# Kernel optimization log

Hardware: AMD Instinct MI355X
Metric: run time of the kernel (lower is better)

Reference implementation:

```python
import jax, jax.numpy as jnp
import numpy as np

B, C = 8, 8
IMG_H, IMG_W = 512, 1280
MAXDISP = (12, 3, 3)
CH3D = (16, 4, 4)          # channels_3d * growth_rate[i]
LAYERS_3D = 4
BASELINE, FOCAL = 0.2, 320.0
MIN_DEPTH, MAX_DEPTH = 0.1, 100.0


def _conv3d(x, w):
    # x: [B,Cin,D,H,W], w: [Cout,Cin,3,3,3], stride 1, padding 1 -> SAME
    return jax.lax.conv_general_dilated(
        x, w, (1, 1, 1), 'SAME',
        dimension_numbers=('NCDHW', 'OIDHW', 'NCDHW'))


def post_3dconv(cost, w_in, w_mid, w_out):
    # cost: [B,1,D,H,W]; conv->relu stack, final conv back to 1 channel
    x = jax.nn.relu(_conv3d(cost, w_in))
    for k in range(w_mid.shape[0]):
        x = jax.nn.relu(_conv3d(x, w_mid[k]))
    return _conv3d(x, w_out)


def build_volume_2d(fl, fr, maxdisp):
    # L1 cost volume: cost[b,d,h,w] = sum_c |fl[...,w] - fr[...,w-d]|, fr zero-padded left
    Bn, Cn, H, W = fl.shape
    d = jnp.arange(maxdisp)
    src = jnp.arange(W)[None, :] - d[:, None]              # [D,W]
    valid = (src >= 0).astype(fl.dtype)
    fr_s = jnp.take(fr, jnp.clip(src, 0, W - 1), axis=3)   # [B,C,H,D,W]
    fr_s = fr_s * valid[None, None, None]
    cost = jnp.abs(fl[:, :, :, None, :] - fr_s).sum(1)     # [B,H,D,W]
    return jnp.transpose(cost, (0, 2, 1, 3))               # [B,D,H,W]


def build_volume_2d3(fl, fr, maxdisp, disp):
    # residual cost volume around current disparity; warp == horizontal bilinear
    # sampling of fr at x - (disp - shift) with zero padding
    Bn, Cn, H, W = fl.shape
    shifts = jnp.arange(-maxdisp + 1, maxdisp, dtype=fl.dtype)      # [S]
    sd = disp[:, 0][:, None] - shifts[None, :, None, None]          # [B,S,H,W]
    xs = jnp.arange(W, dtype=fl.dtype)[None, None, None, :] - sd   # [B,S,H,W]
    x0 = jnp.floor(xs)
    w1 = xs - x0
    x0i = x0.astype(jnp.int32)

    def sample(xi):
        inb = ((xi >= 0) & (xi <= W - 1)).astype(fl.dtype)
        idx = jnp.clip(xi, 0, W - 1)[:, :, None]                    # [B,S,1,H,W]
        v = jnp.take_along_axis(fr[:, None], idx, axis=-1)          # [B,S,C,H,W]
        return v * inb[:, :, None]

    v = sample(x0i) * (1.0 - w1)[:, :, None] + sample(x0i + 1) * w1[:, :, None]
    return jnp.abs(fl[:, None] - v).sum(2)                          # [B,S,H,W]


def disp_reg(cost, start, end):
    p = jax.nn.softmax(-cost, axis=1)
    d = jnp.arange(start, end, dtype=cost.dtype)[None, :, None, None]
    return jnp.sum(p * d, axis=1, keepdims=True)                    # [B,1,H,W]


def upsample(x, h, w):
    Bn, Cn = x.shape[0], x.shape[1]
    return jax.image.resize(x, (Bn, Cn, h, w), method='bilinear')


def _forward(feats_l, feats_r, params, img_h, img_w):
    pred = []
    for s in range(3):
        fl, fr = feats_l[s], feats_r[s]
        H, W = fl.shape[2], fl.shape[3]
        if s == 0:
            cost = build_volume_2d(fl, fr, MAXDISP[0])
        else:
            wflow = upsample(pred[-1], H, W) * (float(H) / img_h)
            cost = build_volume_2d3(fl, fr, MAXDISP[s], wflow)
        cost = post_3dconv(cost[:, None], *params[s])[:, 0]
        if s == 0:
            d = disp_reg(cost, 0, MAXDISP[0])
        else:
            d = disp_reg(cost, -MAXDISP[s] + 1, MAXDISP[s])
        d = d * (img_h / float(H))
        d_up = upsample(d, img_h, img_w)
        pred.append(d_up if s == 0 else d_up + pred[-1])
    disp = jnp.abs(pred[0])
    depth = jnp.nan_to_num(BASELINE * FOCAL / disp,
                           nan=MAX_DEPTH, posinf=MAX_DEPTH, neginf=MIN_DEPTH)
    depth = jnp.clip(depth, MIN_DEPTH, MAX_DEPTH)
    return pred[0], pred[1], pred[2], depth


def setup_inputs() -> dict:
    key = jax.random.key(0)
    ks = jax.random.split(key, 32)
    ki = iter(range(32))

    def feat(h, w):
        return jax.random.normal(ks[next(ki)], (B, C, h, w), jnp.float32)

    inp = {
        'f_l0': feat(IMG_H // 16, IMG_W // 16), 'f_r0': feat(IMG_H // 16, IMG_W // 16),
        'f_l1': feat(IMG_H // 8, IMG_W // 8),   'f_r1': feat(IMG_H // 8, IMG_W // 8),
        'f_l2': feat(IMG_H // 4, IMG_W // 4),   'f_r2': feat(IMG_H // 4, IMG_W // 4),
    }

    def conv_w(o, i):
        n = 27 * o  # kaiming: 3*3*3*out_channels
        return jax.random.normal(ks[next(ki)], (o, i, 3, 3, 3), jnp.float32) * np.float32(np.sqrt(2.0 / n))

    for s, ch in enumerate(CH3D):
        inp[f'w_in{s}'] = conv_w(ch, 1)
        inp[f'w_mid{s}'] = jnp.stack([conv_w(ch, ch) for _ in range(LAYERS_3D)])
        inp[f'w_out{s}'] = conv_w(1, ch)
    inp['img_h'] = IMG_H
    inp['img_w'] = IMG_W
    return inp


def reference(f_l0, f_r0, f_l1, f_r1, f_l2, f_r2,
              w_in0, w_mid0, w_out0,
              w_in1, w_mid1, w_out1,
              w_in2, w_mid2, w_out2,
              img_h, img_w):
    feats_l = (f_l0, f_l1, f_l2)
    feats_r = (f_r0, f_r1, f_r2)
    params = ((w_in0, w_mid0, w_out0), (w_in1, w_mid1, w_out1), (w_in2, w_mid2, w_out2))
    return _forward(feats_l, feats_r, params, img_h, img_w)
```

## Files before the change

### kernel.cpp

```cpp
#include <hip/hip_runtime.h>
#include <math.h>


#define FULL_H 512
#define FULL_W 1280
#define NB 8
#define NPIX (NB * FULL_H * FULL_W)

__global__ __launch_bounds__(256) void cost0_k(const float* __restrict__ fl,
                                               const float* __restrict__ fr,
                                               float* __restrict__ cost) {
    const int H = 32, W = 80, D = 12, C = 8;
    int idx = blockIdx.x * 256 + threadIdx.x;
    int total = NB * D * H * W;
    if (idx >= total) return;
    int w = idx % W; int t = idx / W;
    int h = t % H; t /= H;
    int d = t % D; int b = t / D;
    int src = w - d;
    float acc = 0.f;
    for (int c = 0; c < C; ++c) {
        int base = ((b * C + c) * H + h) * W;
        float flv = fl[base + w];
        float frv = (src >= 0) ? fr[base + src] : 0.f;
        acc += fabsf(flv - frv);
    }
    cost[((b * D + d) * H + h) * W + w] = acc;
}

__global__ __launch_bounds__(256) void costres_k(const float* __restrict__ fl,
                                                 const float* __restrict__ fr,
                                                 const float* __restrict__ wf,
                                                 float* __restrict__ cost,
                                                 int H, int W) {
    const int C = 8, S = 5;
    int idx = blockIdx.x * 256 + threadIdx.x;
    int total = NB * S * H * W;
    if (idx >= total) return;
    int w = idx % W; int t = idx / W;
    int h = t % H; t /= H;
    int s = t % S; int b = t / S;
    float disp  = wf[(b * H + h) * W + w];
    float shift = (float)(s - 2);
    float xs  = (float)w - (disp - shift);
    float x0f = floorf(xs);
    float w1  = xs - x0f;
    float x0fc = fminf(fmaxf(x0f, -2.f), (float)W);
    int x0 = (int)x0fc;
    int x1 = x0 + 1;
    float m0 = (x0 >= 0 && x0 <= W - 1) ? (1.f - w1) : 0.f;
    float m1 = (x1 >= 0 && x1 <= W - 1) ? w1 : 0.f;
    int x0c = min(max(x0, 0), W - 1);
    int x1c = min(max(x1, 0), W - 1);
    float acc = 0.f;
    const float* flb = fl + ((b * C) * H + h) * W;
    const float* frb = fr + ((b * C) * H + h) * W;
    for (int c = 0; c < C; ++c) {
        float v = frb[x0c] * m0 + frb[x1c] * m1;
        acc += fabsf(flb[w] - v);
        flb += H * W;
        frb += H * W;
    }
    cost[idx] = acc;
}

template <int CIN, int COUT, int WT, bool RELU>
__global__ __launch_bounds__(256) void conv2_k(const float* __restrict__ x,
                                               const float* __restrict__ wg,
                                               float* __restrict__ y,
                                               int D, int H, int W, int nstrips) {
    __shared__ __align__(16) float wl[CIN * 27 * COUT];
    for (int i = threadIdx.x; i < CIN * 27 * COUT; i += 256) {
        int co = i % COUT; int rest = i / COUT;
        int tap = rest % 27; int ci = rest / 27;
        wl[i] = wg[(co * CIN + ci) * 27 + tap];
    }
    __syncthreads();

    int idx = blockIdx.x * 256 + threadIdx.x;
    if (idx >= nstrips) return;
    const int SW = W / WT;
    int sw = idx % SW; int t = idx / SW;
    int h = t % H; t /= H;
    int d = t % D; int b = t / D;
    const int wbase = sw * WT;
    const int chs = D * H * W;

    float acc[COUT][WT];
#pragma unroll
    for (int co = 0; co < COUT; ++co)
#pragma unroll
        for (int wt = 0; wt < WT; ++wt) acc[co][wt] = 0.f;

    const bool has_lo = (wbase > 0);
    const bool has_hi = (wbase + WT < W);
    const float* xb = x + (size_t)b * CIN * chs;

    for (int ci = 0; ci < CIN; ++ci) {
        const float* xc = xb + ci * chs;
#pragma unroll
        for (int kd = 0; kd < 3; ++kd) {
            int dd = d + kd - 1; if (dd < 0 || dd >= D) continue;
#pragma unroll
            for (int kh = 0; kh < 3; ++kh) {
                int hh = h + kh - 1; if (hh < 0 || hh >= H) continue;
                const float* row = xc + (dd * H + hh) * W + wbase;
                float xr[WT + 2];
#pragma unroll
                for (int j = 0; j < WT / 4; ++j) {
                    float4 v = *reinterpret_cast<const float4*>(row + j * 4);
                    xr[1 + j * 4 + 0] = v.x; xr[1 + j * 4 + 1] = v.y;
                    xr[1 + j * 4 + 2] = v.z; xr[1 + j * 4 + 3] = v.w;
                }
                xr[0]      = has_lo ? row[-1] : 0.f;
                xr[WT + 1] = has_hi ? row[WT] : 0.f;
                const int tapbase = ci * 27 + kd * 9 + kh * 3;
#pragma unroll
                for (int kw = 0; kw < 3; ++kw) {
                    const float* wp = &wl[(tapbase + kw) * COUT];
                    if constexpr (COUT == 1) {
                        float wv = wp[0];
#pragma unroll
                        for (int wt = 0; wt < WT; ++wt)
                            acc[0][wt] = fmaf(xr[wt + kw], wv, acc[0][wt]);
                    } else {
                        float4 w4[COUT / 4];
#pragma unroll
                        for (int q = 0; q < COUT / 4; ++q)
                            w4[q] = reinterpret_cast<const float4*>(wp)[q];
#pragma unroll
                        for (int wt = 0; wt < WT; ++wt) {
                            float xv = xr[wt + kw];
#pragma unroll
                            for (int q = 0; q < COUT / 4; ++q) {
                                acc[q * 4 + 0][wt] = fmaf(xv, w4[q].x, acc[q * 4 + 0][wt]);
                                acc[q * 4 + 1][wt] = fmaf(xv, w4[q].y, acc[q * 4 + 1][wt]);
                                acc[q * 4 + 2][wt] = fmaf(xv, w4[q].z, acc[q * 4 + 2][wt]);
                                acc[q * 4 + 3][wt] = fmaf(xv, w4[q].w, acc[q * 4 + 3][wt]);
                            }
                        }
                    }
                }
            }
        }
    }

    float* yb = y + (size_t)b * COUT * chs + (d * H + h) * W + wbase;
#pragma unroll
    for (int co = 0; co < COUT; ++co) {
#pragma unroll
        for (int j = 0; j < WT / 4; ++j) {
            float4 v;
            v.x = acc[co][j * 4 + 0]; v.y = acc[co][j * 4 + 1];
            v.z = acc[co][j * 4 + 2]; v.w = acc[co][j * 4 + 3];
            if (RELU) {
                v.x = fmaxf(v.x, 0.f); v.y = fmaxf(v.y, 0.f);
                v.z = fmaxf(v.z, 0.f); v.w = fmaxf(v.w, 0.f);
            }
            *reinterpret_cast<float4*>(yb + co * chs + j * 4) = v;
        }
    }
}

__global__ __launch_bounds__(256) void dispreg_k(const float* __restrict__ cost,
                                                 float* __restrict__ dsm,
                                                 int total, int D, int HW,
                                                 float dstart, float scale) {
    int idx = blockIdx.x * 256 + threadIdx.x;
    if (idx >= total) return;
    int hw = idx % HW; int b = idx / HW;
    const float* c = cost + b * D * HW + hw;
    float m = -1e30f;
    for (int d = 0; d < D; ++d) m = fmaxf(m, -c[d * HW]);
    float s = 0.f, ws = 0.f;
    for (int d = 0; d < D; ++d) {
        float e = expf(-c[d * HW] - m);
        s += e;
        ws = fmaf(e, dstart + (float)d, ws);
    }
    dsm[idx] = ws / s * scale;
}

__global__ __launch_bounds__(256) void upsample_add_k(const float* __restrict__ s,
                                                      int sh, int sw,
                                                      const float* __restrict__ prev,
                                                      float* __restrict__ out) {
    int idx = blockIdx.x * 256 + threadIdx.x;
    if (idx >= NPIX) return;
    int x = idx % FULL_W; int t = idx / FULL_W;
    int y = t % FULL_H; int b = t / FULL_H;
    float fy = (y + 0.5f) * ((float)sh / FULL_H) - 0.5f;
    float fx = (x + 0.5f) * ((float)sw / FULL_W) - 0.5f;
    int y0 = (int)floorf(fy); float wy = fy - (float)y0;
    int x0 = (int)floorf(fx); float wx = fx - (float)x0;
    int y0c = min(max(y0, 0), sh - 1), y1c = min(max(y0 + 1, 0), sh - 1);
    int x0c = min(max(x0, 0), sw - 1), x1c = min(max(x0 + 1, 0), sw - 1);
    const float* sb = s + b * sh * sw;
    float v00 = sb[y0c * sw + x0c], v01 = sb[y0c * sw + x1c];
    float v10 = sb[y1c * sw + x0c], v11 = sb[y1c * sw + x1c];
    float v = (1.f - wy) * ((1.f - wx) * v00 + wx * v01) +
              wy        * ((1.f - wx) * v10 + wx * v11);
    if (prev) v += prev[idx];
    out[idx] = v;
}

__global__ __launch_bounds__(256) void wflow_k(const float* __restrict__ pred,
                                               float* __restrict__ wf,
                                               int oh, int ow, int f, float scale) {
    int idx = blockIdx.x * 256 + threadIdx.x;
    int total = NB * oh * ow;
    if (idx >= total) return;
    int ox = idx % ow; int t = idx / ow;
    int oy = t % oh; int b = t / oh;
    float ff = (float)f, invf = 1.f / (float)f;
    float cy = (oy + 0.5f) * ff - 0.5f;
    float cx = (ox + 0.5f) * ff - 0.5f;
    int ylo = max((int)ceilf(cy - ff), 0);
    int yhi = min((int)floorf(cy + ff), FULL_H - 1);
    int xlo = max((int)ceilf(cx - ff), 0);
    int xhi = min((int)floorf(cx + ff), FULL_W - 1);
    const float* pb = pred + b * FULL_H * FULL_W;
    float acc = 0.f, wys = 0.f, wxs = 0.f;
    for (int iy = ylo; iy <= yhi; ++iy) {
        float wy = 1.f - fabsf((float)iy - cy) * invf;
        wys += wy;
        float rowacc = 0.f;
        const float* row = pb + iy * FULL_W;
        for (int ix = xlo; ix <= xhi; ++ix) {
            float wx = 1.f - fabsf((float)ix - cx) * invf;
            rowacc = fmaf(wx, row[ix], rowacc);
        }
        acc = fmaf(wy, rowacc, acc);
    }
    for (int ix = xlo; ix <= xhi; ++ix) wxs += 1.f - fabsf((float)ix - cx) * invf;
    wf[idx] = acc / (wys * wxs) * scale;
}

__global__ __launch_bounds__(256) void depth_k(const float* __restrict__ pred0,
                                               float* __restrict__ depth) {
    int idx = blockIdx.x * 256 + threadIdx.x;
    if (idx >= NPIX) return;
    float p = fabsf(pred0[idx]);
    float d = 64.f / p;
    if (isnan(d)) d = 100.f;
    d = fminf(fmaxf(d, 0.1f), 100.f);
    depth[idx] = d;
}

static inline dim3 g(int n) { return dim3((n + 255) / 256); }

extern "C" void kernel_launch(void* const* d_in, const int* in_sizes, int n_in,
                              void* d_out, int out_size, void* d_ws, size_t ws_size,
                              hipStream_t stream) {
    const float* f_l0  = (const float*)d_in[0];
    const float* f_r0  = (const float*)d_in[1];
    const float* f_l1  = (const float*)d_in[2];
    const float* f_r1  = (const float*)d_in[3];
    const float* f_l2  = (const float*)d_in[4];
    const float* f_r2  = (const float*)d_in[5];
    const float* w_in0  = (const float*)d_in[6];
    const float* w_mid0 = (const float*)d_in[7];
    const float* w_out0 = (const float*)d_in[8];
    const float* w_in1  = (const float*)d_in[9];
    const float* w_mid1 = (const float*)d_in[10];
    const float* w_out1 = (const float*)d_in[11];
    const float* w_in2  = (const float*)d_in[12];
    const float* w_mid2 = (const float*)d_in[13];
    const float* w_out2 = (const float*)d_in[14];

    float* out   = (float*)d_out;
    float* pred0 = out;
    float* pred1 = out + NPIX;
    float* pred2 = out + 2 * NPIX;
    float* depth = out + 3 * NPIX;

    float* ws   = (float*)d_ws;
    float* xA   = ws;
    float* xB   = xA + 6553600;
    float* cost = xB + 6553600;
    float* dsm  = cost + 1638400;
    float* wfl  = dsm + 327680;

    dim3 blk(256);

    {
        const int D = 12, H = 32, W = 80;
        const int total = NB * D * H * W;
        cost0_k<<<g(total), blk, 0, stream>>>(f_l0, f_r0, cost);
        {
            int ns = total / 4;
            conv2_k<1, 16, 4, true><<<g(ns), blk, 0, stream>>>(cost, w_in0, xA, D, H, W, ns);
            const float* src = xA; float* dst = xB;
            for (int k = 0; k < 4; ++k) {
                conv2_k<16, 16, 4, true><<<g(ns), blk, 0, stream>>>(src, w_mid0 + k * 16 * 16 * 27, dst, D, H, W, ns);
                const float* nsrc = dst; dst = (float*)src; src = nsrc;
            }
            int ns1 = total / 8;
            conv2_k<16, 1, 8, false><<<g(ns1), blk, 0, stream>>>(src, w_out0, cost, D, H, W, ns1);
        }
        dispreg_k<<<g(NB * H * W), blk, 0, stream>>>(cost, dsm, NB * H * W, D, H * W, 0.f, 16.f);
        upsample_add_k<<<g(NPIX), blk, 0, stream>>>(dsm, H, W, nullptr, pred0);
    }

    {
        const int D = 5, H = 64, W = 160;
        const int total = NB * D * H * W;
        wflow_k<<<g(NB * H * W), blk, 0, stream>>>(pred0, wfl, H, W, 8, 0.125f);
        costres_k<<<g(total), blk, 0, stream>>>(f_l1, f_r1, wfl, cost, H, W);
        int ns = total / 8;
        conv2_k<1, 4, 8, true><<<g(ns), blk, 0, stream>>>(cost, w_in1, xA, D, H, W, ns);
        const float* src = xA; float* dst = xB;
        for (int k = 0; k < 4; ++k) {
            conv2_k<4, 4, 8, true><<<g(ns), blk, 0, stream>>>(src, w_mid1 + k * 4 * 4 * 27, dst, D, H, W, ns);
            const float* nsrc = dst; dst = (float*)src; src = nsrc;
        }
        conv2_k<4, 1, 8, false><<<g(ns), blk, 0, stream>>>(src, w_out1, cost, D, H, W, ns);
        dispreg_k<<<g(NB * H * W), blk, 0, stream>>>(cost, dsm, NB * H * W, D, H * W, -2.f, 8.f);
        upsample_add_k<<<g(NPIX), blk, 0, stream>>>(dsm, H, W, pred0, pred1);
    }

    {
        const int D = 5, H = 128, W = 320;
        const int total = NB * D * H * W;
        wflow_k<<<g(NB * H * W), blk, 0, stream>>>(pred1, wfl, H, W, 4, 0.25f);
        costres_k<<<g(total), blk, 0, stream>>>(f_l2, f_r2, wfl, cost, H, W);
        int ns = total / 8;
        conv2_k<1, 4, 8, true><<<g(ns), blk, 0, stream>>>(cost, w_in2, xA, D, H, W, ns);
        const float* src = xA; float* dst = xB;
        for (int k = 0; k < 4; ++k) {
            conv2_k<4, 4, 8, true><<<g(ns), blk, 0, stream>>>(src, w_mid2 + k * 4 * 4 * 27, dst, D, H, W, ns);
            const float* nsrc = dst; dst = (float*)src; src = nsrc;
        }
        conv2_k<4, 1, 8, false><<<g(ns), blk, 0, stream>>>(src, w_out2, cost, D, H, W, ns);
        dispreg_k<<<g(NB * H * W), blk, 0, stream>>>(cost, dsm, NB * H * W, D, H * W, -2.f, 4.f);
        upsample_add_k<<<g(NPIX), blk, 0, stream>>>(dsm, H, W, pred1, pred2);
    }

    depth_k<<<g(NPIX), blk, 0, stream>>>(pred0, depth);
}
```

Before: 1.046 ms.

## Split conv output channels across blocks and fuse depth into upsample

The 3D conv kernel now splits output channels across blocks, so each thread computes fewer output channels. This raises the thread count and cuts per-thread register pressure, at the cost of re-reading the input once per channel group. Strip widths are retuned per stage (WT 4 for stages 0 and 1). The separate depth kernel is folded into the first upsample kernel, which removes one full-resolution pass over pred0.

```diff
diff --git a/kernel.cpp b/kernel.cpp
--- a/kernel.cpp
+++ b/kernel.cpp
@@ -64,20 +64,25 @@
     cost[idx] = acc;
 }
 
-template <int CIN, int COUT, int WT, bool RELU>
-__global__ __launch_bounds__(256) void conv2_k(const float* __restrict__ x,
+template <int CIN, int COUTT, int COUTS, int WT, bool RELU>
+__global__ __launch_bounds__(256) void conv3_k(const float* __restrict__ x,
                                                const float* __restrict__ wg,
                                                float* __restrict__ y,
                                                int D, int H, int W, int nstrips) {
-    __shared__ __align__(16) float wl[CIN * 27 * COUT];
-    for (int i = threadIdx.x; i < CIN * 27 * COUT; i += 256) {
-        int co = i % COUT; int rest = i / COUT;
+    constexpr int NSPL = COUTT / COUTS;
+    int cog, sb;
+    if constexpr (NSPL > 1) { cog = blockIdx.x % NSPL; sb = blockIdx.x / NSPL; }
+    else { cog = 0; sb = blockIdx.x; }
+
+    __shared__ __align__(16) float wl[CIN * 27 * COUTS];
+    for (int i = threadIdx.x; i < CIN * 27 * COUTS; i += 256) {
+        int co = i % COUTS; int rest = i / COUTS;
         int tap = rest % 27; int ci = rest / 27;
-        wl[i] = wg[(co * CIN + ci) * 27 + tap];
+        wl[i] = wg[((cog * COUTS + co) * CIN + ci) * 27 + tap];
     }
     __syncthreads();
 
-    int idx = blockIdx.x * 256 + threadIdx.x;
+    int idx = sb * 256 + threadIdx.x;
     if (idx >= nstrips) return;
     const int SW = W / WT;
     int sw = idx % SW; int t = idx / SW;
@@ -86,9 +91,9 @@
     const int wbase = sw * WT;
     const int chs = D * H * W;
 
-    float acc[COUT][WT];
-#pragma unroll
-    for (int co = 0; co < COUT; ++co)
+    float acc[COUTS][WT];
+#pragma unroll
+    for (int co = 0; co < COUTS; ++co)
 #pragma unroll
         for (int wt = 0; wt < WT; ++wt) acc[co][wt] = 0.f;
 
@@ -117,22 +122,30 @@
                 const int tapbase = ci * 27 + kd * 9 + kh * 3;
 #pragma unroll
                 for (int kw = 0; kw < 3; ++kw) {
-                    const float* wp = &wl[(tapbase + kw) * COUT];
-                    if constexpr (COUT == 1) {
+                    const float* wp = &wl[(tapbase + kw) * COUTS];
+                    if constexpr (COUTS == 1) {
                         float wv = wp[0];
 #pragma unroll
                         for (int wt = 0; wt < WT; ++wt)
                             acc[0][wt] = fmaf(xr[wt + kw], wv, acc[0][wt]);
-                    } else {
-                        float4 w4[COUT / 4];
-#pragma unroll
-                        for (int q = 0; q < COUT / 4; ++q)
-                            w4[q] = reinterpret_cast<const float4*>(wp)[q];
+                    } else if constexpr (COUTS == 2) {
+                        float2 w2 = *reinterpret_cast<const float2*>(wp);
 #pragma unroll
                         for (int wt = 0; wt < WT; ++wt) {
                             float xv = xr[wt + kw];
-#pragma unroll
-                            for (int q = 0; q < COUT / 4; ++q) {
+                            acc[0][wt] = fmaf(xv, w2.x, acc[0][wt]);
+                            acc[1][wt] = fmaf(xv, w2.y, acc[1][wt]);
+                        }
+                    } else {
+                        float4 w4[COUTS / 4];
+#pragma unroll
+                        for (int q = 0; q < COUTS / 4; ++q)
+                            w4[q] = reinterpret_cast<const float4*>(wp)[q];
+#pragma unroll
+                        for (int wt = 0; wt < WT; ++wt) {
+                            float xv = xr[wt + kw];
+#pragma unroll
+                            for (int q = 0; q < COUTS / 4; ++q) {
                                 acc[q * 4 + 0][wt] = fmaf(xv, w4[q].x, acc[q * 4 + 0][wt]);
                                 acc[q * 4 + 1][wt] = fmaf(xv, w4[q].y, acc[q * 4 + 1][wt]);
                                 acc[q * 4 + 2][wt] = fmaf(xv, w4[q].z, acc[q * 4 + 2][wt]);
@@ -145,9 +158,9 @@
         }
     }
 
-    float* yb = y + (size_t)b * COUT * chs + (d * H + h) * W + wbase;
-#pragma unroll
-    for (int co = 0; co < COUT; ++co) {
+    float* yb = y + (size_t)b * COUTT * chs + (size_t)cog * COUTS * chs + (d * H + h) * W + wbase;
+#pragma unroll
+    for (int co = 0; co < COUTS; ++co) {
 #pragma unroll
         for (int j = 0; j < WT / 4; ++j) {
             float4 v;
@@ -184,7 +197,8 @@
 __global__ __launch_bounds__(256) void upsample_add_k(const float* __restrict__ s,
                                                       int sh, int sw,
                                                       const float* __restrict__ prev,
-                                                      float* __restrict__ out) {
+                                                      float* __restrict__ out,
+                                                      float* __restrict__ dep) {
     int idx = blockIdx.x * 256 + threadIdx.x;
     if (idx >= NPIX) return;
     int x = idx % FULL_W; int t = idx / FULL_W;
@@ -202,6 +216,13 @@
               wy        * ((1.f - wx) * v10 + wx * v11);
     if (prev) v += prev[idx];
     out[idx] = v;
+    if (dep) {
+        float p = fabsf(v);
+        float d = 64.f / p;
+        if (isnan(d)) d = 100.f;
+        d = fminf(fmaxf(d, 0.1f), 100.f);
+        dep[idx] = d;
+    }
 }
 
 __global__ __launch_bounds__(256) void wflow_k(const float* __restrict__ pred,
@@ -236,18 +257,8 @@
     wf[idx] = acc / (wys * wxs) * scale;
 }
 
-__global__ __launch_bounds__(256) void depth_k(const float* __restrict__ pred0,
-                                               float* __restrict__ depth) {
-    int idx = blockIdx.x * 256 + threadIdx.x;
-    if (idx >= NPIX) return;
-    float p = fabsf(pred0[idx]);
-    float d = 64.f / p;
-    if (isnan(d)) d = 100.f;
-    d = fminf(fmaxf(d, 0.1f), 100.f);
-    depth[idx] = d;
-}
-
 static inline dim3 g(int n) { return dim3((n + 255) / 256); }
+static inline dim3 gs(int nstrips, int nspl) { return dim3(((nstrips + 255) / 256) * nspl); }
 
 extern "C" void kernel_launch(void* const* d_in, const int* in_sizes, int n_in,
                               void* d_out, int out_size, void* d_ws, size_t ws_size,
@@ -287,19 +298,16 @@
         const int D = 12, H = 32, W = 80;
         const int total = NB * D * H * W;
         cost0_k<<<g(total), blk, 0, stream>>>(f_l0, f_r0, cost);
-        {
-            int ns = total / 4;
-            conv2_k<1, 16, 4, true><<<g(ns), blk, 0, stream>>>(cost, w_in0, xA, D, H, W, ns);
-            const float* src = xA; float* dst = xB;
-            for (int k = 0; k < 4; ++k) {
-                conv2_k<16, 16, 4, true><<<g(ns), blk, 0, stream>>>(src, w_mid0 + k * 16 * 16 * 27, dst, D, H, W, ns);
-                const float* nsrc = dst; dst = (float*)src; src = nsrc;
-            }
-            int ns1 = total / 8;
-            conv2_k<16, 1, 8, false><<<g(ns1), blk, 0, stream>>>(src, w_out0, cost, D, H, W, ns1);
-        }
+        int ns4 = total / 4;
+        conv3_k<1, 16, 4, 4, true><<<gs(ns4, 4), blk, 0, stream>>>(cost, w_in0, xA, D, H, W, ns4);
+        const float* src = xA; float* dst = xB;
+        for (int k = 0; k < 4; ++k) {
+            conv3_k<16, 16, 2, 4, true><<<gs(ns4, 8), blk, 0, stream>>>(src, w_mid0 + k * 16 * 16 * 27, dst, D, H, W, ns4);
+            const float* nsrc = dst; dst = (float*)src; src = nsrc;
+        }
+        conv3_k<16, 1, 1, 4, false><<<gs(ns4, 1), blk, 0, stream>>>(src, w_out0, cost, D, H, W, ns4);
         dispreg_k<<<g(NB * H * W), blk, 0, stream>>>(cost, dsm, NB * H * W, D, H * W, 0.f, 16.f);
-        upsample_add_k<<<g(NPIX), blk, 0, stream>>>(dsm, H, W, nullptr, pred0);
+        upsample_add_k<<<g(NPIX), blk, 0, stream>>>(dsm, H, W, nullptr, pred0, depth);
     }
 
     {
@@ -307,16 +315,16 @@
         const int total = NB * D * H * W;
         wflow_k<<<g(NB * H * W), blk, 0, stream>>>(pred0, wfl, H, W, 8, 0.125f);
         costres_k<<<g(total), blk, 0, stream>>>(f_l1, f_r1, wfl, cost, H, W);
-        int ns = total / 8;
-        conv2_k<1, 4, 8, true><<<g(ns), blk, 0, stream>>>(cost, w_in1, xA, D, H, W, ns);
+        int ns4 = total / 4;
+        conv3_k<1, 4, 2, 4, true><<<gs(ns4, 2), blk, 0, stream>>>(cost, w_in1, xA, D, H, W, ns4);
         const float* src = xA; float* dst = xB;
         for (int k = 0; k < 4; ++k) {
-            conv2_k<4, 4, 8, true><<<g(ns), blk, 0, stream>>>(src, w_mid1 + k * 4 * 4 * 27, dst, D, H, W, ns);
+            conv3_k<4, 4, 2, 4, true><<<gs(ns4, 2), blk, 0, stream>>>(src, w_mid1 + k * 4 * 4 * 27, dst, D, H, W, ns4);
             const float* nsrc = dst; dst = (float*)src; src = nsrc;
         }
-        conv2_k<4, 1, 8, false><<<g(ns), blk, 0, stream>>>(src, w_out1, cost, D, H, W, ns);
+        conv3_k<4, 1, 1, 4, false><<<gs(ns4, 1), blk, 0, stream>>>(src, w_out1, cost, D, H, W, ns4);
         dispreg_k<<<g(NB * H * W), blk, 0, stream>>>(cost, dsm, NB * H * W, D, H * W, -2.f, 8.f);
-        upsample_add_k<<<g(NPIX), blk, 0, stream>>>(dsm, H, W, pred0, pred1);
+        upsample_add_k<<<g(NPIX), blk, 0, stream>>>(dsm, H, W, pred0, pred1, nullptr);
     }
 
     {
@@ -324,17 +332,15 @@
         const int total = NB * D * H * W;
         wflow_k<<<g(NB * H * W), blk, 0, stream>>>(pred1, wfl, H, W, 4, 0.25f);
         costres_k<<<g(total), blk, 0, stream>>>(f_l2, f_r2, wfl, cost, H, W);
-        int ns = total / 8;
-        conv2_k<1, 4, 8, true><<<g(ns), blk, 0, stream>>>(cost, w_in2, xA, D, H, W, ns);
+        int ns8 = total / 8;
+        conv3_k<1, 4, 2, 8, true><<<gs(ns8, 2), blk, 0, stream>>>(cost, w_in2, xA, D, H, W, ns8);
         const float* src = xA; float* dst = xB;
         for (int k = 0; k < 4; ++k) {
-            conv2_k<4, 4, 8, true><<<g(ns), blk, 0, stream>>>(src, w_mid2 + k * 4 * 4 * 27, dst, D, H, W, ns);
+            conv3_k<4, 4, 2, 8, true><<<gs(ns8, 2), blk, 0, stream>>>(src, w_mid2 + k * 4 * 4 * 27, dst, D, H, W, ns8);
             const float* nsrc = dst; dst = (float*)src; src = nsrc;
         }
-        conv2_k<4, 1, 8, false><<<g(ns), blk, 0, stream>>>(src, w_out2, cost, D, H, W, ns);
+        conv3_k<4, 1, 1, 8, false><<<gs(ns8, 1), blk, 0, stream>>>(src, w_out2, cost, D, H, W, ns8);
         dispreg_k<<<g(NB * H * W), blk, 0, stream>>>(cost, dsm, NB * H * W, D, H * W, -2.f, 4.f);
-        upsample_add_k<<<g(NPIX), blk, 0, stream>>>(dsm, H, W, pred1, pred2);
-    }
-
-    depth_k<<<g(NPIX), blk, 0, stream>>>(pred0, depth);
-}
+        upsample_add_k<<<g(NPIX), blk, 0, stream>>>(dsm, H, W, pred1, pred2, nullptr);
+    }
+}
```

Measured after the change: 1.533 ms. 46.6% more time.

## Use zero-padded activation buffers for 3D convs and fuse depth into upsample

Applied to the files above, without the earlier changes.

Stores cost volumes and intermediate activations in zero-padded halo layouts, so the conv kernel reads neighbours without boundary checks or skipped taps. The padded buffers are cleared with memsets before each stage. Depth computation is folded into the first upsample kernel, which removes one full-resolution pass, and the stage-1 tile width drops to 4 for more threads. The cost is extra memset traffic and larger buffers, in exchange for branch-free, fully unrolled inner loops.

```diff
diff --git a/kernel.cpp b/kernel.cpp
--- a/kernel.cpp
+++ b/kernel.cpp
@@ -7,10 +7,11 @@
 #define NB 8
 #define NPIX (NB * FULL_H * FULL_W)
 
-__global__ __launch_bounds__(256) void cost0_k(const float* __restrict__ fl,
-                                               const float* __restrict__ fr,
-                                               float* __restrict__ cost) {
+__global__ __launch_bounds__(256) void cost0p_k(const float* __restrict__ fl,
+                                                const float* __restrict__ fr,
+                                                float* __restrict__ costp) {
     const int H = 32, W = 80, D = 12, C = 8;
+    const int DZ = 14, HZ = 34, WZ = 88;
     int idx = blockIdx.x * 256 + threadIdx.x;
     int total = NB * D * H * W;
     if (idx >= total) return;
@@ -25,15 +26,15 @@
         float frv = (src >= 0) ? fr[base + src] : 0.f;
         acc += fabsf(flv - frv);
     }
-    cost[((b * D + d) * H + h) * W + w] = acc;
-}
-
-__global__ __launch_bounds__(256) void costres_k(const float* __restrict__ fl,
-                                                 const float* __restrict__ fr,
-                                                 const float* __restrict__ wf,
-                                                 float* __restrict__ cost,
-                                                 int H, int W) {
-    const int C = 8, S = 5;
+    costp[((b * DZ + (d + 1)) * HZ + (h + 1)) * WZ + (w + 4)] = acc;
+}
+
+__global__ __launch_bounds__(256) void costresp_k(const float* __restrict__ fl,
+                                                  const float* __restrict__ fr,
+                                                  const float* __restrict__ wf,
+                                                  float* __restrict__ costp,
+                                                  int H, int W, int HZ, int WZ) {
+    const int C = 8, S = 5, DZ = 7;
     int idx = blockIdx.x * 256 + threadIdx.x;
     int total = NB * S * H * W;
     if (idx >= total) return;
@@ -61,14 +62,16 @@
         flb += H * W;
         frb += H * W;
     }
-    cost[idx] = acc;
-}
-
-template <int CIN, int COUT, int WT, bool RELU>
-__global__ __launch_bounds__(256) void conv2_k(const float* __restrict__ x,
+    costp[((b * DZ + (s + 1)) * HZ + (h + 1)) * WZ + (w + 4)] = acc;
+}
+
+template <int CIN, int COUT, int WT, bool RELU, bool PADOUT>
+__global__ __launch_bounds__(256) void convp_k(const float* __restrict__ x,
                                                const float* __restrict__ wg,
                                                float* __restrict__ y,
-                                               int D, int H, int W, int nstrips) {
+                                               int D, int H, int W,
+                                               int DZ, int HZ, int WZ,
+                                               int nstrips) {
     __shared__ __align__(16) float wl[CIN * 27 * COUT];
     for (int i = threadIdx.x; i < CIN * 27 * COUT; i += 256) {
         int co = i % COUT; int rest = i / COUT;
@@ -83,8 +86,9 @@
     int sw = idx % SW; int t = idx / SW;
     int h = t % H; t /= H;
     int d = t % D; int b = t / D;
-    const int wbase = sw * WT;
-    const int chs = D * H * W;
+    const int wcol = sw * WT + 4;
+    const int zhs = HZ * WZ;
+    const int zcs = DZ * zhs;
 
     float acc[COUT][WT];
 #pragma unroll
@@ -92,19 +96,15 @@
 #pragma unroll
         for (int wt = 0; wt < WT; ++wt) acc[co][wt] = 0.f;
 
-    const bool has_lo = (wbase > 0);
-    const bool has_hi = (wbase + WT < W);
-    const float* xb = x + (size_t)b * CIN * chs;
+    const float* xb = x + (size_t)b * CIN * zcs + (size_t)d * zhs + (size_t)h * WZ + wcol;
 
     for (int ci = 0; ci < CIN; ++ci) {
-        const float* xc = xb + ci * chs;
+        const float* xc = xb + (size_t)ci * zcs;
 #pragma unroll
         for (int kd = 0; kd < 3; ++kd) {
-            int dd = d + kd - 1; if (dd < 0 || dd >= D) continue;
 #pragma unroll
             for (int kh = 0; kh < 3; ++kh) {
-                int hh = h + kh - 1; if (hh < 0 || hh >= H) continue;
-                const float* row = xc + (dd * H + hh) * W + wbase;
+                const float* row = xc + kd * zhs + kh * WZ;
                 float xr[WT + 2];
 #pragma unroll
                 for (int j = 0; j < WT / 4; ++j) {
@@ -112,8 +112,8 @@
                     xr[1 + j * 4 + 0] = v.x; xr[1 + j * 4 + 1] = v.y;
                     xr[1 + j * 4 + 2] = v.z; xr[1 + j * 4 + 3] = v.w;
                 }
-                xr[0]      = has_lo ? row[-1] : 0.f;
-                xr[WT + 1] = has_hi ? row[WT] : 0.f;
+                xr[0]      = row[-1];
+                xr[WT + 1] = row[WT];
                 const int tapbase = ci * 27 + kd * 9 + kh * 3;
 #pragma unroll
                 for (int kw = 0; kw < 3; ++kw) {
@@ -145,19 +145,38 @@
         }
     }
 
-    float* yb = y + (size_t)b * COUT * chs + (d * H + h) * W + wbase;
-#pragma unroll
-    for (int co = 0; co < COUT; ++co) {
-#pragma unroll
-        for (int j = 0; j < WT / 4; ++j) {
-            float4 v;
-            v.x = acc[co][j * 4 + 0]; v.y = acc[co][j * 4 + 1];
-            v.z = acc[co][j * 4 + 2]; v.w = acc[co][j * 4 + 3];
-            if (RELU) {
-                v.x = fmaxf(v.x, 0.f); v.y = fmaxf(v.y, 0.f);
-                v.z = fmaxf(v.z, 0.f); v.w = fmaxf(v.w, 0.f);
+    if constexpr (PADOUT) {
+        float* yb = y + (size_t)b * COUT * zcs + (size_t)(d + 1) * zhs + (size_t)(h + 1) * WZ + wcol;
+#pragma unroll
+        for (int co = 0; co < COUT; ++co) {
+#pragma unroll
+            for (int j = 0; j < WT / 4; ++j) {
+                float4 v;
+                v.x = acc[co][j * 4 + 0]; v.y = acc[co][j * 4 + 1];
+                v.z = acc[co][j * 4 + 2]; v.w = acc[co][j * 4 + 3];
+                if (RELU) {
+                    v.x = fmaxf(v.x, 0.f); v.y = fmaxf(v.y, 0.f);
+                    v.z = fmaxf(v.z, 0.f); v.w = fmaxf(v.w, 0.f);
+                }
+                *reinterpret_cast<float4*>(yb + (size_t)co * zcs + j * 4) = v;
             }
-            *reinterpret_cast<float4*>(yb + co * chs + j * 4) = v;
+        }
+    } else {
+        const int chs = D * H * W;
+        float* yb = y + (size_t)b * COUT * chs + (d * H + h) * W + sw * WT;
+#pragma unroll
+        for (int co = 0; co < COUT; ++co) {
+#pragma unroll
+            for (int j = 0; j < WT / 4; ++j) {
+                float4 v;
+                v.x = acc[co][j * 4 + 0]; v.y = acc[co][j * 4 + 1];
+                v.z = acc[co][j * 4 + 2]; v.w = acc[co][j * 4 + 3];
+                if (RELU) {
+                    v.x = fmaxf(v.x, 0.f); v.y = fmaxf(v.y, 0.f);
+                    v.z = fmaxf(v.z, 0.f); v.w = fmaxf(v.w, 0.f);
+                }
+                *reinterpret_cast<float4*>(yb + (size_t)co * chs + j * 4) = v;
+            }
         }
     }
 }
@@ -184,7 +203,8 @@
 __global__ __launch_bounds__(256) void upsample_add_k(const float* __restrict__ s,
                                                       int sh, int sw,
                                                       const float* __restrict__ prev,
-                                                      float* __restrict__ out) {
+                                                      float* __restrict__ out,
+                                                      float* __restrict__ dep) {
     int idx = blockIdx.x * 256 + threadIdx.x;
     if (idx >= NPIX) return;
     int x = idx % FULL_W; int t = idx / FULL_W;
@@ -202,6 +222,13 @@
               wy        * ((1.f - wx) * v10 + wx * v11);
     if (prev) v += prev[idx];
     out[idx] = v;
+    if (dep) {
+        float p = fabsf(v);
+        float d = 64.f / p;
+        if (isnan(d)) d = 100.f;
+        d = fminf(fmaxf(d, 0.1f), 100.f);
+        dep[idx] = d;
+    }
 }
 
 __global__ __launch_bounds__(256) void wflow_k(const float* __restrict__ pred,
@@ -236,17 +263,6 @@
     wf[idx] = acc / (wys * wxs) * scale;
 }
 
-__global__ __launch_bounds__(256) void depth_k(const float* __restrict__ pred0,
-                                               float* __restrict__ depth) {
-    int idx = blockIdx.x * 256 + threadIdx.x;
-    if (idx >= NPIX) return;
-    float p = fabsf(pred0[idx]);
-    float d = 64.f / p;
-    if (isnan(d)) d = 100.f;
-    d = fminf(fmaxf(d, 0.1f), 100.f);
-    depth[idx] = d;
-}
-
 static inline dim3 g(int n) { return dim3((n + 255) / 256); }
 
 extern "C" void kernel_launch(void* const* d_in, const int* in_sizes, int n_in,
@@ -274,67 +290,80 @@
     float* pred2 = out + 2 * NPIX;
     float* depth = out + 3 * NPIX;
 
-    float* ws   = (float*)d_ws;
-    float* xA   = ws;
-    float* xB   = xA + 6553600;
-    float* cost = xB + 6553600;
-    float* dsm  = cost + 1638400;
-    float* wfl  = dsm + 327680;
+    float* ws = (float*)d_ws;
+    float* P    = ws;
+    float* Q    = ws + 9551360;
+    float* CP   = ws + 19102720;
+    float* CO   = ws + 21490560;
+    float* dsm  = ws + 23128960;
+    float* wfl  = ws + 23456640;
 
     dim3 blk(256);
 
     {
-        const int D = 12, H = 32, W = 80;
+        const int D = 12, H = 32, W = 80, DZ = 14, HZ = 34, WZ = 88;
+        const size_t pcn = (size_t)NB * 16 * DZ * HZ * WZ;
+        const size_t cpn = (size_t)NB * DZ * HZ * WZ;
+        hipMemsetAsync(P,  0, pcn * 4, stream);
+        hipMemsetAsync(Q,  0, pcn * 4, stream);
+        hipMemsetAsync(CP, 0, cpn * 4, stream);
         const int total = NB * D * H * W;
-        cost0_k<<<g(total), blk, 0, stream>>>(f_l0, f_r0, cost);
-        {
-            int ns = total / 4;
-            conv2_k<1, 16, 4, true><<<g(ns), blk, 0, stream>>>(cost, w_in0, xA, D, H, W, ns);
-            const float* src = xA; float* dst = xB;
-            for (int k = 0; k < 4; ++k) {
-                conv2_k<16, 16, 4, true><<<g(ns), blk, 0, stream>>>(src, w_mid0 + k * 16 * 16 * 27, dst, D, H, W, ns);
-                const float* nsrc = dst; dst = (float*)src; src = nsrc;
-            }
-            int ns1 = total / 8;
-            conv2_k<16, 1, 8, false><<<g(ns1), blk, 0, stream>>>(src, w_out0, cost, D, H, W, ns1);
-        }
-        dispreg_k<<<g(NB * H * W), blk, 0, stream>>>(cost, dsm, NB * H * W, D, H * W, 0.f, 16.f);
-        upsample_add_k<<<g(NPIX), blk, 0, stream>>>(dsm, H, W, nullptr, pred0);
+        cost0p_k<<<g(total), blk, 0, stream>>>(f_l0, f_r0, CP);
+        int ns4 = total / 4;
+        int ns8 = total / 8;
+        convp_k<1, 16, 4, true, true><<<g(ns4), blk, 0, stream>>>(CP, w_in0, P, D, H, W, DZ, HZ, WZ, ns4);
+        const float* src = P; float* dst = Q;
+        for (int k = 0; k < 4; ++k) {
+            convp_k<16, 16, 4, true, true><<<g(ns4), blk, 0, stream>>>(src, w_mid0 + k * 16 * 16 * 27, dst, D, H, W, DZ, HZ, WZ, ns4);
+            const float* nsrc = dst; dst = (float*)src; src = nsrc;
+        }
+        convp_k<16, 1, 8, false, false><<<g(ns8), blk, 0, stream>>>(src, w_out0, CO, D, H, W, DZ, HZ, WZ, ns8);
+        dispreg_k<<<g(NB * H * W), blk, 0, stream>>>(CO, dsm, NB * H * W, D, H * W, 0.f, 16.f);
+        upsample_add_k<<<g(NPIX), blk, 0, stream>>>(dsm, H, W, nullptr, pred0, depth);
     }
 
     {
-        const int D = 5, H = 64, W = 160;
+        const int D = 5, H = 64, W = 160, DZ = 7, HZ = 66, WZ = 168;
+        const size_t pcn = (size_t)NB * 4 * DZ * HZ * WZ;
+        const size_t cpn = (size_t)NB * DZ * HZ * WZ;
+        hipMemsetAsync(P,  0, pcn * 4, stream);
+        hipMemsetAsync(Q,  0, pcn * 4, stream);
+        hipMemsetAsync(CP, 0, cpn * 4, stream);
         const int total = NB * D * H * W;
         wflow_k<<<g(NB * H * W), blk, 0, stream>>>(pred0, wfl, H, W, 8, 0.125f);
-        costres_k<<<g(total), blk, 0, stream>>>(f_l1, f_r1, wfl, cost, H, W);
-        int ns = total / 8;
-        conv2_k<1, 4, 8, true><<<g(ns), blk, 0, stream>>>(cost, w_in1, xA, D, H, W, ns);
-        const float* src = xA; float* dst = xB;
+        costresp_k<<<g(total), blk, 0, stream>>>(f_l1, f_r1, wfl, CP, H, W, HZ, WZ);
+        int ns4 = total / 4;
+        int ns8 = total / 8;
+        convp_k<1, 4, 4, true, true><<<g(ns4), blk, 0, stream>>>(CP, w_in1, P, D, H, W, DZ, HZ, WZ, ns4);
+        const float* src = P; float* dst = Q;
         for (int k = 0; k < 4; ++k) {
-            conv2_k<4, 4, 8, true><<<g(ns), blk, 0, stream>>>(src, w_mid1 + k * 4 * 4 * 27, dst, D, H, W, ns);
+            convp_k<4, 4, 4, true, true><<<g(ns4), blk, 0, stream>>>(src, w_mid1 + k * 4 * 4 * 27, dst, D, H, W, DZ, HZ, WZ, ns4);
             const float* nsrc = dst; dst = (float*)src; src = nsrc;
         }
-        conv2_k<4, 1, 8, false><<<g(ns), blk, 0, stream>>>(src, w_out1, cost, D, H, W, ns);
-        dispreg_k<<<g(NB * H * W), blk, 0, stream>>>(cost, dsm, NB * H * W, D, H * W, -2.f, 8.f);
-        upsample_add_k<<<g(NPIX), blk, 0, stream>>>(dsm, H, W, pred0, pred1);
+        convp_k<4, 1, 8, false, false><<<g(ns8), blk, 0, stream>>>(src, w_out1, CO, D, H, W, DZ, HZ, WZ, ns8);
+        dispreg_k<<<g(NB * H * W), blk, 0, stream>>>(CO, dsm, NB * H * W, D, H * W, -2.f, 8.f);
+        upsample_add_k<<<g(NPIX), blk, 0, stream>>>(dsm, H, W, pred0, pred1, nullptr);
     }
 
     {
-        const int D = 5, H = 128, W = 320;
+        const int D = 5, H = 128, W = 320, DZ = 7, HZ = 130, WZ = 328;
+        const size_t pcn = (size_t)NB * 4 * DZ * HZ * WZ;
+        const size_t cpn = (size_t)NB * DZ * HZ * WZ;
+        hipMemsetAsync(P,  0, pcn * 4, stream);
+        hipMemsetAsync(Q,  0, pcn * 4, stream);
+        hipMemsetAsync(CP, 0, cpn * 4, stream);
         const int total = NB * D * H * W;
         wflow_k<<<g(NB * H * W), blk, 0, stream>>>(pred1, wfl, H, W, 4, 0.25f);
-        costres_k<<<g(total), blk, 0, stream>>>(f_l2, f_r2, wfl, cost, H, W);
-        int ns = total / 8;
-        conv2_k<1, 4, 8, true><<<g(ns), blk, 0, stream>>>(cost, w_in2, xA, D, H, W, ns);
-        const float* src = xA; float* dst = xB;
+        costresp_k<<<g(total), blk, 0, stream>>>(f_l2, f_r2, wfl, CP, H, W, HZ, WZ);
+        int ns8 = total / 8;
+        convp_k<1, 4, 8, true, true><<<g(ns8), blk, 0, stream>>>(CP, w_in2, P, D, H, W, DZ, HZ, WZ, ns8);
+        const float* src = P; float* dst = Q;
         for (int k = 0; k < 4; ++k) {
-            conv2_k<4, 4, 8, true><<<g(ns), blk, 0, stream>>>(src, w_mid2 + k * 4 * 4 * 27, dst, D, H, W, ns);
+            convp_k<4, 4, 8, true, true><<<g(ns8), blk, 0, stream>>>(src, w_mid2 + k * 4 * 4 * 27, dst, D, H, W, DZ, HZ, WZ, ns8);
             const float* nsrc = dst; dst = (float*)src; src = nsrc;
         }
-        conv2_k<4, 1, 8, false><<<g(ns), blk, 0, stream>>>(src, w_out2, cost, D, H, W, ns);
-        dispreg_k<<<g(NB * H * W), blk, 0, stream>>>(cost, dsm, NB * H * W, D, H * W, -2.f, 4.f);
-        upsample_add_k<<<g(NPIX), blk, 0, stream>>>(dsm, H, W, pred1, pred2);
-    }
-
-    depth_k<<<g(NPIX), blk, 0, stream>>>(pred0, depth);
-}
+        convp_k<4, 1, 8, false, false><<<g(ns8), blk, 0, stream>>>(src, w_out2, CO, D, H, W, DZ, HZ, WZ, ns8);
+        dispreg_k<<<g(NB * H * W), blk, 0, stream>>>(CO, dsm, NB * H * W, D, H * W, -2.f, 4.f);
+        upsample_add_k<<<g(NPIX), blk, 0, stream>>>(dsm, H, W, pred1, pred2, nullptr);
+    }
+}
```

New measurement: 1.063 ms. About the same (+1.6%).
